# Kernel optimization log

Measured on AMD Instinct MI355X. Metric: run time of the kernel, lower is better.

The kernel has to match this reference:

```python
import jax, jax.numpy as jnp
import numpy as np

N = 100000        # nodes
E = 1600000       # edges (avg degree 16)
F_IN = 128        # num_node_features
H = 64            # hidden_channels
F_EDGE = 8        # num_edge_features (output dim per edge)


def setup_inputs() -> dict:
    key = jax.random.key(0)
    ks = jax.random.split(key, 9)
    x = jax.random.normal(ks[0], (N, F_IN), dtype=jnp.float32)
    edge_index = jax.random.randint(ks[1], (2, E), 0, N, dtype=jnp.int32)
    s = 0.05
    W1 = jax.random.normal(ks[2], (F_IN, H), jnp.float32) * s
    b1 = jnp.zeros((H,), jnp.float32)
    W2 = jax.random.normal(ks[3], (H, H), jnp.float32) * s
    b2 = jnp.zeros((H,), jnp.float32)
    Wl = jax.random.normal(ks[4], (2 * H, F_EDGE), jnp.float32) * s
    bl = jnp.zeros((F_EDGE,), jnp.float32)
    return {"x": x, "edge_index": edge_index,
            "W1": W1, "b1": b1, "W2": W2, "b2": b2, "Wl": Wl, "bl": bl}


def gcn_conv(x, W, b, row, col, n):
    # GCNConv: h = D^{-1/2} (A + I) D^{-1/2} (x W) + b
    h = x @ W
    sl = jnp.arange(n, dtype=row.dtype)          # self-loops
    r = jnp.concatenate([row, sl])
    c = jnp.concatenate([col, sl])
    ones = jnp.ones(r.shape[0], dtype=h.dtype)
    deg = jax.ops.segment_sum(ones, c, num_segments=n)      # in-degree incl. self-loop
    dinv = jax.lax.rsqrt(jnp.maximum(deg, 1e-12))
    norm = dinv[r] * dinv[c]                                 # symmetric normalization
    agg = jax.ops.segment_sum(norm[:, None] * h[r], c, num_segments=n)
    return agg + b


def reference(x, edge_index, W1, b1, W2, b2, Wl, bl):
    row, col = edge_index[0], edge_index[1]
    h = jax.nn.relu(gcn_conv(x, W1, b1, row, col, N))
    # dropout p=0.5 is identity at inference (training=False)
    h = jax.nn.relu(gcn_conv(h, W2, b2, row, col, N))
    x_i = h[row]                                  # [E, H]
    x_j = h[col]                                  # [E, H]
    return jnp.concatenate([x_i, x_j], axis=-1) @ Wl + bl   # [E, F_EDGE]
```

## Files before the change

kernel.cpp:

```cpp
#include <hip/hip_runtime.h>
#include <hip/hip_bf16.h>

static constexpr int NN  = 100000;
static constexpr int NE  = 1600000;
static constexpr int FIN = 128;
static constexpr int HD  = 64;

static constexpr int NB    = 256;
static constexpr int NPB   = 392;
static constexpr int EPB   = NE / NB;
static constexpr unsigned long long DIV392_MAGIC = 43826197ULL;

typedef __attribute__((ext_vector_type(8))) short bf16x8;
typedef __attribute__((ext_vector_type(4))) float f32x4;

__device__ __forceinline__ float bf2f(unsigned short u) {
    return __uint_as_float(((unsigned int)u) << 16);
}
__device__ __forceinline__ unsigned short f2bf(float f) {
    __hip_bfloat16 hb = __float2bfloat16(f);
    return *(unsigned short*)&hb;
}
__device__ __forceinline__ int bucket_of(int c) {
    return (int)(((unsigned long long)(unsigned int)c * DIV392_MAGIC) >> 34);
}

__global__ __launch_bounds__(256) void k_detect(const unsigned short* __restrict__ xu,
                                                int* __restrict__ flag) {
    __shared__ int sd[256];
    int t = threadIdx.x;
    int cnt = 0;
    for (int k = t; k < 4096; k += 256) {
        unsigned short u = xu[2 * k];
        int ex = (u >> 7) & 0xFF;
        cnt += (ex >= 110 && ex <= 135) ? 1 : 0;
    }
    sd[t] = cnt;
    __syncthreads();
    for (int off = 128; off > 0; off >>= 1) {
        if (t < off) sd[t] += sd[t + off];
        __syncthreads();
    }
    if (t == 0) flag[0] = (sd[0] >= 2048) ? 1 : 0;
}

__device__ __forceinline__ float load_in(const void* p, size_t i, int isbf) {
    return isbf ? bf2f(((const unsigned short*)p)[i]) : ((const float*)p)[i];
}

__global__ __launch_bounds__(256) void k_hist(const int* __restrict__ col, int* __restrict__ hist) {
    __shared__ int h[4][NB];
    int t = threadIdx.x, w = t >> 6;
#pragma unroll
    for (int r = 0; r < 4; ++r) h[r][t] = 0;
    __syncthreads();
    int base = blockIdx.x * EPB;
    for (int e = base + t; e < base + EPB; e += 256)
        atomicAdd(&h[w][bucket_of(col[e])], 1);
    __syncthreads();
    hist[t * NB + blockIdx.x] = h[0][t] + h[1][t] + h[2][t] + h[3][t];
}

__global__ __launch_bounds__(256) void k_gscan1(int* __restrict__ a, int* __restrict__ bsums) {
    __shared__ int sd[256];
    int t = threadIdx.x;
    int base = blockIdx.x * 1024 + t * 4;
    int v0 = a[base], v1 = a[base + 1], v2 = a[base + 2], v3 = a[base + 3];
    int tsum = v0 + v1 + v2 + v3;
    sd[t] = tsum;
    __syncthreads();
    for (int off = 1; off < 256; off <<= 1) {
        int tmp = (t >= off) ? sd[t - off] : 0;
        __syncthreads();
        sd[t] += tmp;
        __syncthreads();
    }
    int run = sd[t] - tsum;
    a[base] = run; run += v0;
    a[base + 1] = run; run += v1;
    a[base + 2] = run; run += v2;
    a[base + 3] = run;
    if (t == 255) bsums[blockIdx.x] = sd[t];
}

__global__ __launch_bounds__(256) void k_gscan2(int* __restrict__ bsums) {
    __shared__ int sd[256];
    int t = threadIdx.x;
    int v = (t < 64) ? bsums[t] : 0;
    sd[t] = v;
    __syncthreads();
    for (int off = 1; off < 256; off <<= 1) {
        int tmp = (t >= off) ? sd[t - off] : 0;
        __syncthreads();
        sd[t] += tmp;
        __syncthreads();
    }
    if (t < 64) bsums[t] = sd[t] - v;
}

__global__ __launch_bounds__(256) void k_binfill(const int* __restrict__ row, const int* __restrict__ col,
                                                 const int* __restrict__ histS, const int* __restrict__ bsums,
                                                 int* __restrict__ csr_tmp) {
    __shared__ int cur[NB];
    int t = threadIdx.x;
    cur[t] = histS[t * NB + blockIdx.x] + bsums[t >> 2];
    __syncthreads();
    int base = blockIdx.x * EPB;
    for (int e = base + t; e < base + EPB; e += 256) {
        int r = row[e], c = col[e];
        int b = bucket_of(c);
        int p = atomicAdd(&cur[b], 1);
        csr_tmp[p] = r | ((c - b * NPB) << 17);
    }
}

__global__ __launch_bounds__(256) void k_bsort(const int* __restrict__ csr_tmp,
                                               const int* __restrict__ histS,
                                               const int* __restrict__ bsums,
                                               int* __restrict__ csr_src,
                                               int* __restrict__ start,
                                               float* __restrict__ dinv) {
    __shared__ int cnt[512];
    __shared__ int cur[512];
    int t = threadIdx.x;
    int k = blockIdx.x;
    int S = histS[k * NB] + bsums[k >> 2];
    int E = (k < NB - 1) ? (histS[(k + 1) * NB] + bsums[(k + 1) >> 2]) : NE;
    int nbase = k * NPB;
    cnt[t] = 0; cnt[t + 256] = 0;
    __syncthreads();
    for (int e = S + t; e < E; e += 256)
        atomicAdd(&cnt[csr_tmp[e] >> 17], 1);
    __syncthreads();
    int rc0 = cnt[t], rc1 = cnt[t + 256];
    for (int d = 1; d < 512; d <<= 1) {
        int idx = (t + 1) * (d << 1) - 1;
        if (idx < 512) cnt[idx] += cnt[idx - d];
        __syncthreads();
    }
    if (t == 0) cnt[511] = 0;
    __syncthreads();
    for (int d = 256; d >= 1; d >>= 1) {
        int idx = (t + 1) * (d << 1) - 1;
        if (idx < 512) { int tmp = cnt[idx - d]; cnt[idx - d] = cnt[idx]; cnt[idx] += tmp; }
        __syncthreads();
    }
    int n0 = nbase + t;
    if (n0 < NN) {
        start[n0] = S + cnt[t] + rc0;
        dinv[n0] = rsqrtf((float)(rc0 + 1));
    }
    int li = t + 256;
    int n1 = nbase + li;
    if (li < NPB && n1 < NN) {
        start[n1] = S + cnt[li] + rc1;
        dinv[n1] = rsqrtf((float)(rc1 + 1));
    }
    cur[t] = cnt[t]; cur[t + 256] = cnt[t + 256];
    __syncthreads();
    for (int e = S + t; e < E; e += 256) {
        int u = csr_tmp[e];
        int p = atomicAdd(&cur[u >> 17], 1);
        csr_src[S + p] = u & 0x1FFFF;
    }
}

template <int K, bool XDUAL>
__global__ __launch_bounds__(256) void k_gemm_mfma(const void* __restrict__ X,
                                                   const void* __restrict__ W,
                                                   const float* __restrict__ dinv,
                                                   unsigned short* __restrict__ T0,
                                                   unsigned short* __restrict__ T1,
                                                   const int* __restrict__ flag) {
    constexpr int KT = K / 32;
    __shared__ unsigned short Bs[KT * 4 * 64 * 8];
    int isbf = flag[0];
    for (int tup = threadIdx.x; tup < KT * 4 * 64; tup += 256) {
        int l  = tup & 63;
        int nt = (tup >> 6) & 3;
        int kt = tup >> 8;
        int n  = nt * 16 + (l & 15);
        int kb = kt * 32 + (l >> 4) * 8;
        unsigned short tmp[8];
#pragma unroll
        for (int j = 0; j < 8; ++j) tmp[j] = f2bf(load_in(W, (size_t)(kb + j) * HD + n, isbf));
        *((uint4*)&Bs[(size_t)tup * 8]) = *((const uint4*)tmp);
    }
    __syncthreads();
    int wave = threadIdx.x >> 6, lane = threadIdx.x & 63;
    int quad = lane >> 4, m = lane & 15;
    int row0 = blockIdx.x * 64 + wave * 16;
    int row  = row0 + m;
    int rowc = (row < NN) ? row : (NN - 1);
    bool xf32 = XDUAL && (isbf == 0);
    const char* xrow = (const char*)X + (size_t)rowc * K * (xf32 ? 4 : 2);
    f32x4 acc[4];
#pragma unroll
    for (int nt = 0; nt < 4; ++nt) acc[nt] = (f32x4){0.f, 0.f, 0.f, 0.f};
#pragma unroll
    for (int kt = 0; kt < KT; ++kt) {
        bf16x8 a;
        if (!xf32) {
            a = *((const bf16x8*)(xrow + (size_t)(kt * 32 + quad * 8) * 2));
        } else {
            const float4* fp = (const float4*)(xrow + (size_t)(kt * 32 + quad * 8) * 4);
            float4 u0 = fp[0], u1 = fp[1];
            unsigned short tmp[8] = {f2bf(u0.x), f2bf(u0.y), f2bf(u0.z), f2bf(u0.w),
                                     f2bf(u1.x), f2bf(u1.y), f2bf(u1.z), f2bf(u1.w)};
            a = *((const bf16x8*)tmp);
        }
#pragma unroll
        for (int nt = 0; nt < 4; ++nt) {
            bf16x8 b = *((const bf16x8*)&Bs[(size_t)((kt * 4 + nt) * 64 + lane) * 8]);
            acc[nt] = __builtin_amdgcn_mfma_f32_16x16x32_bf16(a, b, acc[nt], 0, 0, 0);
        }
    }
#pragma unroll
    for (int r = 0; r < 4; ++r) {
        int orow = row0 + quad * 4 + r;
        if (orow < NN) {
            float sc = dinv[orow];
#pragma unroll
            for (int nt = 0; nt < 4; ++nt) {
                unsigned short* Th = (nt >= 2) ? T1 : T0;
                Th[(size_t)orow * 32 + (nt & 1) * 16 + m] = f2bf(acc[nt][r] * sc);
            }
        }
    }
}

__global__ __launch_bounds__(256) void k_agg_half(const unsigned short* __restrict__ Th,
                                                  unsigned short* __restrict__ Hout,
                                                  const int* __restrict__ endOff,
                                                  const int* __restrict__ csr_src,
                                                  const float* __restrict__ dinv,
                                                  const void* __restrict__ bias,
                                                  const int* __restrict__ flag,
                                                  int half) {
    int isbf = flag[0];
    int lane = threadIdx.x & 63, wave = threadIdx.x >> 6;
    int g  = lane >> 3;
    int fl = (lane & 7) * 4;
    int i = blockIdx.x * 32 + wave * 8 + g;
    int end = endOff[i];
    int beg = (i == 0) ? 0 : endOff[i - 1];
    float a0, a1, a2, a3;
    {
        ushort4 t = *((const ushort4*)(Th + (size_t)i * 32 + fl));
        a0 = bf2f(t.x); a1 = bf2f(t.y); a2 = bf2f(t.z); a3 = bf2f(t.w);
    }
    int k = beg;
    for (; k + 3 < end; k += 4) {
        int s0 = csr_src[k], s1 = csr_src[k + 1], s2 = csr_src[k + 2], s3 = csr_src[k + 3];
        ushort4 t0 = *((const ushort4*)(Th + (size_t)s0 * 32 + fl));
        ushort4 t1 = *((const ushort4*)(Th + (size_t)s1 * 32 + fl));
        ushort4 t2 = *((const ushort4*)(Th + (size_t)s2 * 32 + fl));
        ushort4 t3 = *((const ushort4*)(Th + (size_t)s3 * 32 + fl));
        a0 += bf2f(t0.x) + bf2f(t1.x) + bf2f(t2.x) + bf2f(t3.x);
        a1 += bf2f(t0.y) + bf2f(t1.y) + bf2f(t2.y) + bf2f(t3.y);
        a2 += bf2f(t0.z) + bf2f(t1.z) + bf2f(t2.z) + bf2f(t3.z);
        a3 += bf2f(t0.w) + bf2f(t1.w) + bf2f(t2.w) + bf2f(t3.w);
    }
    for (; k < end; ++k) {
        int s = csr_src[k];
        ushort4 t = *((const ushort4*)(Th + (size_t)s * 32 + fl));
        a0 += bf2f(t.x); a1 += bf2f(t.y); a2 += bf2f(t.z); a3 += bf2f(t.w);
    }
    float di = dinv[i];
    int fg = half * 32 + fl;
    float b0 = load_in(bias, fg + 0, isbf), b1 = load_in(bias, fg + 1, isbf);
    float b2 = load_in(bias, fg + 2, isbf), b3 = load_in(bias, fg + 3, isbf);
    ushort4 o;
    o.x = f2bf(fmaxf(fmaf(di, a0, b0), 0.f));
    o.y = f2bf(fmaxf(fmaf(di, a1, b1), 0.f));
    o.z = f2bf(fmaxf(fmaf(di, a2, b2), 0.f));
    o.w = f2bf(fmaxf(fmaf(di, a3, b3), 0.f));
    *((ushort4*)(Hout + (size_t)i * HD + fg)) = o;
}

__global__ __launch_bounds__(256) void k_pgemm(const __hip_bfloat16* __restrict__ H,
                                               const void* __restrict__ Wl,
                                               const void* __restrict__ bl,
                                               unsigned short* __restrict__ P,
                                               const int* __restrict__ flag) {
    int isbf = flag[0];
    int wave = threadIdx.x >> 6, lane = threadIdx.x & 63;
    int quad = lane >> 4, m = lane & 15;
    bf16x8 bfr[2];
#pragma unroll
    for (int kt = 0; kt < 2; ++kt) {
        unsigned short tmp[8];
#pragma unroll
        for (int j = 0; j < 8; ++j) {
            int kk = kt * 32 + quad * 8 + j;
            float w = (m < 8) ? load_in(Wl, (size_t)kk * 8 + m, isbf)
                              : load_in(Wl, (size_t)(64 + kk) * 8 + (m - 8), isbf);
            tmp[j] = f2bf(w);
        }
        bfr[kt] = *((const bf16x8*)tmp);
    }
    float binit = (m < 8) ? load_in(bl, m, isbf) : 0.f;
    int row0 = blockIdx.x * 64 + wave * 16;
    int row  = row0 + m;
    int rowc = (row < NN) ? row : (NN - 1);
    const __hip_bfloat16* hrow = H + (size_t)rowc * HD;
    bf16x8 x0 = *((const bf16x8*)(hrow + quad * 8));
    bf16x8 x1 = *((const bf16x8*)(hrow + 32 + quad * 8));
    f32x4 acc = (f32x4){binit, binit, binit, binit};
    acc = __builtin_amdgcn_mfma_f32_16x16x32_bf16(x0, bfr[0], acc, 0, 0, 0);
    acc = __builtin_amdgcn_mfma_f32_16x16x32_bf16(x1, bfr[1], acc, 0, 0, 0);
#pragma unroll
    for (int r = 0; r < 4; ++r) {
        int orow = row0 + quad * 4 + r;
        if (orow < NN) P[(size_t)orow * 16 + m] = f2bf(acc[r]);
    }
}

__global__ __launch_bounds__(256) void k_edge_add(const unsigned short* __restrict__ P,
                                                  const int* __restrict__ erow,
                                                  const int* __restrict__ ecol,
                                                  void* __restrict__ out,
                                                  const int* __restrict__ flag) {
    int isbf = flag[0];
    int e = blockIdx.x * 256 + threadIdx.x;
    int i = erow[e], j = ecol[e];
    ushort4 r0 = *((const ushort4*)(P + (size_t)i * 16));
    ushort4 r1 = *((const ushort4*)(P + (size_t)i * 16 + 4));
    ushort4 c0 = *((const ushort4*)(P + (size_t)j * 16 + 8));
    ushort4 c1 = *((const ushort4*)(P + (size_t)j * 16 + 12));
    float v[8] = {bf2f(r0.x) + bf2f(c0.x), bf2f(r0.y) + bf2f(c0.y),
                  bf2f(r0.z) + bf2f(c0.z), bf2f(r0.w) + bf2f(c0.w),
                  bf2f(r1.x) + bf2f(c1.x), bf2f(r1.y) + bf2f(c1.y),
                  bf2f(r1.z) + bf2f(c1.z), bf2f(r1.w) + bf2f(c1.w)};
    if (isbf) {
        union { unsigned short h[8]; uint4 u; } p;
#pragma unroll
        for (int o = 0; o < 8; ++o) p.h[o] = f2bf(v[o]);
        *((uint4*)((__hip_bfloat16*)out + (size_t)e * 8)) = p.u;
    } else {
        float* op = (float*)out + (size_t)e * 8;
        ((float4*)op)[0] = make_float4(v[0], v[1], v[2], v[3]);
        ((float4*)op)[1] = make_float4(v[4], v[5], v[6], v[7]);
    }
}

extern "C" void kernel_launch(void* const* d_in, const int* in_sizes, int n_in,
                              void* d_out, int out_size, void* d_ws, size_t ws_size,
                              hipStream_t stream) {
    const void* x  = d_in[0];
    const int*  ei = (const int*)d_in[1];
    const void* W1 = d_in[2];
    const void* b1 = d_in[3];
    const void* W2 = d_in[4];
    const void* b2 = d_in[5];
    const void* Wl = d_in[6];
    const void* bl = d_in[7];
    const int* row = ei;
    const int* col = ei + NE;

    char* ws = (char*)d_ws;
    int*   flag    = (int*)ws;    ws += 16;
    int*   hist    = (int*)ws;    ws += (size_t)NB * NB * 4;
    int*   bsums   = (int*)ws;    ws += 256 * 4;
    int*   start   = (int*)ws;    ws += (size_t)NN * 4;
    float* dinv    = (float*)ws;  ws += (size_t)NN * 4;
    int*   csr_tmp = (int*)ws;    ws += (size_t)NE * 4;
    int*   csr_src = (int*)ws;    ws += (size_t)NE * 4;
    unsigned short* T0 = (unsigned short*)ws;  ws += (size_t)NN * 32 * 2;
    unsigned short* T1 = (unsigned short*)ws;  ws += (size_t)NN * 32 * 2;
    __hip_bfloat16* bufH = (__hip_bfloat16*)ws;  ws += (size_t)NN * HD * 2;
    unsigned short* P = (unsigned short*)ws;

    int gE   = (NE + 255) / 256;
    int gN32 = NN / 32;
    int gN64 = (NN + 63) / 64;

    k_detect<<<1, 256, 0, stream>>>((const unsigned short*)x, flag);
    k_hist   <<<NB, 256, 0, stream>>>(col, hist);
    k_gscan1 <<<64, 256, 0, stream>>>(hist, bsums);
    k_gscan2 <<<1, 256, 0, stream>>>(bsums);
    k_binfill<<<NB, 256, 0, stream>>>(row, col, hist, bsums, csr_tmp);
    k_bsort  <<<NB, 256, 0, stream>>>(csr_tmp, hist, bsums, csr_src, start, dinv);

    k_gemm_mfma<FIN, true><<<gN64, 256, 0, stream>>>(x, W1, dinv, T0, T1, flag);
    k_agg_half<<<gN32, 256, 0, stream>>>(T0, (unsigned short*)bufH, start, csr_src, dinv, b1, flag, 0);
    k_agg_half<<<gN32, 256, 0, stream>>>(T1, (unsigned short*)bufH, start, csr_src, dinv, b1, flag, 1);

    k_gemm_mfma<HD, false><<<gN64, 256, 0, stream>>>(bufH, W2, dinv, T0, T1, flag);
    k_agg_half<<<gN32, 256, 0, stream>>>(T0, (unsigned short*)bufH, start, csr_src, dinv, b2, flag, 0);
    k_agg_half<<<gN32, 256, 0, stream>>>(T1, (unsigned short*)bufH, start, csr_src, dinv, b2, flag, 1);

    k_pgemm<<<gN64, 256, 0, stream>>>(bufH, Wl, bl, P, flag);
    k_edge_add<<<gE, 256, 0, stream>>>(P, row, col, d_out, flag);
}
```

Baseline: 335.0 us.

## Fuse aggregation with following GEMMs and merge small setup kernels

Folds the dtype-detect kernel into the histogram kernel and replaces the block-sum scan kernel with a small in-block scan inside the binfill and bsort kernels. Each GCN aggregation now gathers full 64-wide rows in a single pass instead of two half passes. The aggregated rows are staged in LDS and fed directly to the next MFMA GEMM (W2 or the edge projection), so the intermediate hidden buffer never goes through global memory. This cuts kernel launches and global round trips, at the cost of redundant bsums scans in every block and wider per-lane gathers.

```diff
diff --git a/kernel.cpp b/kernel.cpp
--- a/kernel.cpp
+++ b/kernel.cpp
@@ -25,30 +25,13 @@
     return (int)(((unsigned long long)(unsigned int)c * DIV392_MAGIC) >> 34);
 }
 
-__global__ __launch_bounds__(256) void k_detect(const unsigned short* __restrict__ xu,
-                                                int* __restrict__ flag) {
-    __shared__ int sd[256];
-    int t = threadIdx.x;
-    int cnt = 0;
-    for (int k = t; k < 4096; k += 256) {
-        unsigned short u = xu[2 * k];
-        int ex = (u >> 7) & 0xFF;
-        cnt += (ex >= 110 && ex <= 135) ? 1 : 0;
-    }
-    sd[t] = cnt;
-    __syncthreads();
-    for (int off = 128; off > 0; off >>= 1) {
-        if (t < off) sd[t] += sd[t + off];
-        __syncthreads();
-    }
-    if (t == 0) flag[0] = (sd[0] >= 2048) ? 1 : 0;
-}
-
 __device__ __forceinline__ float load_in(const void* p, size_t i, int isbf) {
     return isbf ? bf2f(((const unsigned short*)p)[i]) : ((const float*)p)[i];
 }
 
-__global__ __launch_bounds__(256) void k_hist(const int* __restrict__ col, int* __restrict__ hist) {
+__global__ __launch_bounds__(256) void k_hist(const int* __restrict__ col, int* __restrict__ hist,
+                                              const unsigned short* __restrict__ xu,
+                                              int* __restrict__ flag) {
     __shared__ int h[4][NB];
     int t = threadIdx.x, w = t >> 6;
 #pragma unroll
@@ -59,6 +42,22 @@
         atomicAdd(&h[w][bucket_of(col[e])], 1);
     __syncthreads();
     hist[t * NB + blockIdx.x] = h[0][t] + h[1][t] + h[2][t] + h[3][t];
+    if (blockIdx.x == 0) {
+        __syncthreads();
+        int cnt = 0;
+        for (int k = t; k < 4096; k += 256) {
+            unsigned short u = xu[2 * k];
+            int ex = (u >> 7) & 0xFF;
+            cnt += (ex >= 110 && ex <= 135) ? 1 : 0;
+        }
+        h[0][t] = cnt;
+        __syncthreads();
+        for (int off = 128; off > 0; off >>= 1) {
+            if (t < off) h[0][t] += h[0][t + off];
+            __syncthreads();
+        }
+        if (t == 0) flag[0] = (h[0][0] >= 2048) ? 1 : 0;
+    }
 }
 
 __global__ __launch_bounds__(256) void k_gscan1(int* __restrict__ a, int* __restrict__ bsums) {
@@ -83,27 +82,30 @@
     if (t == 255) bsums[blockIdx.x] = sd[t];
 }
 
-__global__ __launch_bounds__(256) void k_gscan2(int* __restrict__ bsums) {
-    __shared__ int sd[256];
+__device__ __forceinline__ void scan_bsums(const int* __restrict__ bsumsRaw, int* sb) {
     int t = threadIdx.x;
-    int v = (t < 64) ? bsums[t] : 0;
-    sd[t] = v;
-    __syncthreads();
-    for (int off = 1; off < 256; off <<= 1) {
-        int tmp = (t >= off) ? sd[t - off] : 0;
-        __syncthreads();
-        sd[t] += tmp;
-        __syncthreads();
-    }
-    if (t < 64) bsums[t] = sd[t] - v;
+    int myv = 0;
+    if (t < 64) { myv = bsumsRaw[t]; sb[t] = myv; }
+    __syncthreads();
+    for (int off = 1; off < 64; off <<= 1) {
+        int v = (t < 64 && t >= off) ? sb[t - off] : 0;
+        __syncthreads();
+        if (t < 64) sb[t] += v;
+        __syncthreads();
+    }
+    if (t < 64) sb[t] -= myv;
+    __syncthreads();
 }
 
 __global__ __launch_bounds__(256) void k_binfill(const int* __restrict__ row, const int* __restrict__ col,
-                                                 const int* __restrict__ histS, const int* __restrict__ bsums,
+                                                 const int* __restrict__ histS,
+                                                 const int* __restrict__ bsumsRaw,
                                                  int* __restrict__ csr_tmp) {
     __shared__ int cur[NB];
+    __shared__ int sb[64];
     int t = threadIdx.x;
-    cur[t] = histS[t * NB + blockIdx.x] + bsums[t >> 2];
+    scan_bsums(bsumsRaw, sb);
+    cur[t] = histS[t * NB + blockIdx.x] + sb[t >> 2];
     __syncthreads();
     int base = blockIdx.x * EPB;
     for (int e = base + t; e < base + EPB; e += 256) {
@@ -116,18 +118,20 @@
 
 __global__ __launch_bounds__(256) void k_bsort(const int* __restrict__ csr_tmp,
                                                const int* __restrict__ histS,
-                                               const int* __restrict__ bsums,
+                                               const int* __restrict__ bsumsRaw,
                                                int* __restrict__ csr_src,
                                                int* __restrict__ start,
                                                float* __restrict__ dinv) {
     __shared__ int cnt[512];
     __shared__ int cur[512];
+    __shared__ int sb[64];
     int t = threadIdx.x;
     int k = blockIdx.x;
-    int S = histS[k * NB] + bsums[k >> 2];
-    int E = (k < NB - 1) ? (histS[(k + 1) * NB] + bsums[(k + 1) >> 2]) : NE;
+    cnt[t] = 0; cnt[t + 256] = 0;
+    scan_bsums(bsumsRaw, sb);
+    int S = histS[k * NB] + sb[k >> 2];
+    int E = (k < NB - 1) ? (histS[(k + 1) * NB] + sb[(k + 1) >> 2]) : NE;
     int nbase = k * NPB;
-    cnt[t] = 0; cnt[t + 256] = 0;
     __syncthreads();
     for (int e = S + t; e < E; e += 256)
         atomicAdd(&cnt[csr_tmp[e] >> 17], 1);
@@ -169,8 +173,7 @@
 __global__ __launch_bounds__(256) void k_gemm_mfma(const void* __restrict__ X,
                                                    const void* __restrict__ W,
                                                    const float* __restrict__ dinv,
-                                                   unsigned short* __restrict__ T0,
-                                                   unsigned short* __restrict__ T1,
+                                                   unsigned short* __restrict__ T,
                                                    const int* __restrict__ flag) {
     constexpr int KT = K / 32;
     __shared__ unsigned short Bs[KT * 4 * 64 * 8];
@@ -221,70 +224,118 @@
         if (orow < NN) {
             float sc = dinv[orow];
 #pragma unroll
-            for (int nt = 0; nt < 4; ++nt) {
-                unsigned short* Th = (nt >= 2) ? T1 : T0;
-                Th[(size_t)orow * 32 + (nt & 1) * 16 + m] = f2bf(acc[nt][r] * sc);
-            }
-        }
-    }
-}
-
-__global__ __launch_bounds__(256) void k_agg_half(const unsigned short* __restrict__ Th,
-                                                  unsigned short* __restrict__ Hout,
+            for (int nt = 0; nt < 4; ++nt)
+                T[(size_t)orow * 64 + nt * 16 + m] = f2bf(acc[nt][r] * sc);
+        }
+    }
+}
+
+__device__ __forceinline__ void agg_to_lds(const unsigned short* __restrict__ T,
+                                           const int* __restrict__ endOff,
+                                           const int* __restrict__ csr_src,
+                                           const float* __restrict__ dinv,
+                                           const void* __restrict__ bias, int isbf,
+                                           unsigned short (*hS)[72], int i0) {
+    int lane = threadIdx.x & 63, wave = threadIdx.x >> 6;
+    int g  = lane >> 3;
+    int fl = (lane & 7) * 8;
+    int li = wave * 8 + g;
+    int i  = i0 + li;
+    int end = endOff[i];
+    int beg = (i == 0) ? 0 : endOff[i - 1];
+    union U { uint4 u; unsigned short s[8]; };
+    float a[8];
+    {
+        U t; t.u = *((const uint4*)(T + (size_t)i * 64 + fl));
+#pragma unroll
+        for (int j = 0; j < 8; ++j) a[j] = bf2f(t.s[j]);
+    }
+    int k = beg;
+    for (; k + 3 < end; k += 4) {
+        int s0 = csr_src[k], s1 = csr_src[k + 1], s2 = csr_src[k + 2], s3 = csr_src[k + 3];
+        U t0, t1, t2, t3;
+        t0.u = *((const uint4*)(T + (size_t)s0 * 64 + fl));
+        t1.u = *((const uint4*)(T + (size_t)s1 * 64 + fl));
+        t2.u = *((const uint4*)(T + (size_t)s2 * 64 + fl));
+        t3.u = *((const uint4*)(T + (size_t)s3 * 64 + fl));
+#pragma unroll
+        for (int j = 0; j < 8; ++j)
+            a[j] += bf2f(t0.s[j]) + bf2f(t1.s[j]) + bf2f(t2.s[j]) + bf2f(t3.s[j]);
+    }
+    for (; k < end; ++k) {
+        int s = csr_src[k];
+        U t; t.u = *((const uint4*)(T + (size_t)s * 64 + fl));
+#pragma unroll
+        for (int j = 0; j < 8; ++j) a[j] += bf2f(t.s[j]);
+    }
+    float di = dinv[i];
+    U o;
+#pragma unroll
+    for (int j = 0; j < 8; ++j)
+        o.s[j] = f2bf(fmaxf(fmaf(di, a[j], load_in(bias, fl + j, isbf)), 0.f));
+    *((uint4*)&hS[li][fl]) = o.u;
+}
+
+__global__ __launch_bounds__(256) void k_agg_gemm(const unsigned short* __restrict__ T,
                                                   const int* __restrict__ endOff,
                                                   const int* __restrict__ csr_src,
                                                   const float* __restrict__ dinv,
                                                   const void* __restrict__ bias,
+                                                  const void* __restrict__ W2,
                                                   const int* __restrict__ flag,
-                                                  int half) {
+                                                  unsigned short* __restrict__ Tb) {
+    __shared__ unsigned short hS[32][72];
+    __shared__ unsigned short Bs[2 * 4 * 64 * 8];
     int isbf = flag[0];
-    int lane = threadIdx.x & 63, wave = threadIdx.x >> 6;
-    int g  = lane >> 3;
-    int fl = (lane & 7) * 4;
-    int i = blockIdx.x * 32 + wave * 8 + g;
-    int end = endOff[i];
-    int beg = (i == 0) ? 0 : endOff[i - 1];
-    float a0, a1, a2, a3;
-    {
-        ushort4 t = *((const ushort4*)(Th + (size_t)i * 32 + fl));
-        a0 = bf2f(t.x); a1 = bf2f(t.y); a2 = bf2f(t.z); a3 = bf2f(t.w);
-    }
-    int k = beg;
-    for (; k + 3 < end; k += 4) {
-        int s0 = csr_src[k], s1 = csr_src[k + 1], s2 = csr_src[k + 2], s3 = csr_src[k + 3];
-        ushort4 t0 = *((const ushort4*)(Th + (size_t)s0 * 32 + fl));
-        ushort4 t1 = *((const ushort4*)(Th + (size_t)s1 * 32 + fl));
-        ushort4 t2 = *((const ushort4*)(Th + (size_t)s2 * 32 + fl));
-        ushort4 t3 = *((const ushort4*)(Th + (size_t)s3 * 32 + fl));
-        a0 += bf2f(t0.x) + bf2f(t1.x) + bf2f(t2.x) + bf2f(t3.x);
-        a1 += bf2f(t0.y) + bf2f(t1.y) + bf2f(t2.y) + bf2f(t3.y);
-        a2 += bf2f(t0.z) + bf2f(t1.z) + bf2f(t2.z) + bf2f(t3.z);
-        a3 += bf2f(t0.w) + bf2f(t1.w) + bf2f(t2.w) + bf2f(t3.w);
-    }
-    for (; k < end; ++k) {
-        int s = csr_src[k];
-        ushort4 t = *((const ushort4*)(Th + (size_t)s * 32 + fl));
-        a0 += bf2f(t.x); a1 += bf2f(t.y); a2 += bf2f(t.z); a3 += bf2f(t.w);
-    }
-    float di = dinv[i];
-    int fg = half * 32 + fl;
-    float b0 = load_in(bias, fg + 0, isbf), b1 = load_in(bias, fg + 1, isbf);
-    float b2 = load_in(bias, fg + 2, isbf), b3 = load_in(bias, fg + 3, isbf);
-    ushort4 o;
-    o.x = f2bf(fmaxf(fmaf(di, a0, b0), 0.f));
-    o.y = f2bf(fmaxf(fmaf(di, a1, b1), 0.f));
-    o.z = f2bf(fmaxf(fmaf(di, a2, b2), 0.f));
-    o.w = f2bf(fmaxf(fmaf(di, a3, b3), 0.f));
-    *((ushort4*)(Hout + (size_t)i * HD + fg)) = o;
-}
-
-__global__ __launch_bounds__(256) void k_pgemm(const __hip_bfloat16* __restrict__ H,
-                                               const void* __restrict__ Wl,
-                                               const void* __restrict__ bl,
-                                               unsigned short* __restrict__ P,
-                                               const int* __restrict__ flag) {
+    for (int tup = threadIdx.x; tup < 512; tup += 256) {
+        int l  = tup & 63;
+        int nt = (tup >> 6) & 3;
+        int kt = tup >> 8;
+        int n  = nt * 16 + (l & 15);
+        int kb = kt * 32 + (l >> 4) * 8;
+        unsigned short tmp[8];
+#pragma unroll
+        for (int j = 0; j < 8; ++j) tmp[j] = f2bf(load_in(W2, (size_t)(kb + j) * HD + n, isbf));
+        *((uint4*)&Bs[(size_t)tup * 8]) = *((const uint4*)tmp);
+    }
+    int i0 = blockIdx.x * 32;
+    agg_to_lds(T, endOff, csr_src, dinv, bias, isbf, hS, i0);
+    __syncthreads();
+    int wave = threadIdx.x >> 6, lane = threadIdx.x & 63;
+    int quad = lane >> 4, m = lane & 15;
+    int tile = wave >> 1;
+    int nb   = (wave & 1) * 2;
+    f32x4 acc0 = (f32x4){0.f, 0.f, 0.f, 0.f};
+    f32x4 acc1 = (f32x4){0.f, 0.f, 0.f, 0.f};
+#pragma unroll
+    for (int kt = 0; kt < 2; ++kt) {
+        bf16x8 a  = *((const bf16x8*)&hS[tile * 16 + m][kt * 32 + quad * 8]);
+        bf16x8 b0 = *((const bf16x8*)&Bs[(size_t)((kt * 4 + nb) * 64 + lane) * 8]);
+        bf16x8 b1 = *((const bf16x8*)&Bs[(size_t)((kt * 4 + nb + 1) * 64 + lane) * 8]);
+        acc0 = __builtin_amdgcn_mfma_f32_16x16x32_bf16(a, b0, acc0, 0, 0, 0);
+        acc1 = __builtin_amdgcn_mfma_f32_16x16x32_bf16(a, b1, acc1, 0, 0, 0);
+    }
+#pragma unroll
+    for (int r = 0; r < 4; ++r) {
+        int orow = i0 + tile * 16 + quad * 4 + r;
+        float sc = dinv[orow];
+        Tb[(size_t)orow * 64 + nb * 16 + m]       = f2bf(acc0[r] * sc);
+        Tb[(size_t)orow * 64 + (nb + 1) * 16 + m] = f2bf(acc1[r] * sc);
+    }
+}
+
+__global__ __launch_bounds__(256) void k_agg_pgemm(const unsigned short* __restrict__ T,
+                                                   const int* __restrict__ endOff,
+                                                   const int* __restrict__ csr_src,
+                                                   const float* __restrict__ dinv,
+                                                   const void* __restrict__ bias,
+                                                   const void* __restrict__ Wl,
+                                                   const void* __restrict__ bl,
+                                                   const int* __restrict__ flag,
+                                                   unsigned short* __restrict__ P) {
+    __shared__ unsigned short hS[32][72];
     int isbf = flag[0];
-    int wave = threadIdx.x >> 6, lane = threadIdx.x & 63;
+    int lane = threadIdx.x & 63;
     int quad = lane >> 4, m = lane & 15;
     bf16x8 bfr[2];
 #pragma unroll
@@ -300,19 +351,22 @@
         bfr[kt] = *((const bf16x8*)tmp);
     }
     float binit = (m < 8) ? load_in(bl, m, isbf) : 0.f;
-    int row0 = blockIdx.x * 64 + wave * 16;
-    int row  = row0 + m;
-    int rowc = (row < NN) ? row : (NN - 1);
-    const __hip_bfloat16* hrow = H + (size_t)rowc * HD;
-    bf16x8 x0 = *((const bf16x8*)(hrow + quad * 8));
-    bf16x8 x1 = *((const bf16x8*)(hrow + 32 + quad * 8));
-    f32x4 acc = (f32x4){binit, binit, binit, binit};
-    acc = __builtin_amdgcn_mfma_f32_16x16x32_bf16(x0, bfr[0], acc, 0, 0, 0);
-    acc = __builtin_amdgcn_mfma_f32_16x16x32_bf16(x1, bfr[1], acc, 0, 0, 0);
-#pragma unroll
-    for (int r = 0; r < 4; ++r) {
-        int orow = row0 + quad * 4 + r;
-        if (orow < NN) P[(size_t)orow * 16 + m] = f2bf(acc[r]);
+    int i0 = blockIdx.x * 32;
+    agg_to_lds(T, endOff, csr_src, dinv, bias, isbf, hS, i0);
+    __syncthreads();
+    int wave = threadIdx.x >> 6;
+    if (wave < 2) {
+        f32x4 acc = (f32x4){binit, binit, binit, binit};
+#pragma unroll
+        for (int kt = 0; kt < 2; ++kt) {
+            bf16x8 a = *((const bf16x8*)&hS[wave * 16 + m][kt * 32 + quad * 8]);
+            acc = __builtin_amdgcn_mfma_f32_16x16x32_bf16(a, bfr[kt], acc, 0, 0, 0);
+        }
+#pragma unroll
+        for (int r = 0; r < 4; ++r) {
+            int orow = i0 + wave * 16 + quad * 4 + r;
+            P[(size_t)orow * 16 + m] = f2bf(acc[r]);
+        }
     }
 }
 
@@ -366,30 +420,24 @@
     float* dinv    = (float*)ws;  ws += (size_t)NN * 4;
     int*   csr_tmp = (int*)ws;    ws += (size_t)NE * 4;
     int*   csr_src = (int*)ws;    ws += (size_t)NE * 4;
-    unsigned short* T0 = (unsigned short*)ws;  ws += (size_t)NN * 32 * 2;
-    unsigned short* T1 = (unsigned short*)ws;  ws += (size_t)NN * 32 * 2;
-    __hip_bfloat16* bufH = (__hip_bfloat16*)ws;  ws += (size_t)NN * HD * 2;
-    unsigned short* P = (unsigned short*)ws;
+    unsigned short* T  = (unsigned short*)ws;  ws += (size_t)NN * 64 * 2;
+    unsigned short* Tb = (unsigned short*)ws;  ws += (size_t)NN * 64 * 2;
+    unsigned short* P  = (unsigned short*)ws;
 
     int gE   = (NE + 255) / 256;
     int gN32 = NN / 32;
     int gN64 = (NN + 63) / 64;
 
-    k_detect<<<1, 256, 0, stream>>>((const unsigned short*)x, flag);
-    k_hist   <<<NB, 256, 0, stream>>>(col, hist);
+    k_hist   <<<NB, 256, 0, stream>>>(col, hist, (const unsigned short*)x, flag);
     k_gscan1 <<<64, 256, 0, stream>>>(hist, bsums);
-    k_gscan2 <<<1, 256, 0, stream>>>(bsums);
     k_binfill<<<NB, 256, 0, stream>>>(row, col, hist, bsums, csr_tmp);
     k_bsort  <<<NB, 256, 0, stream>>>(csr_tmp, hist, bsums, csr_src, start, dinv);
 
-    k_gemm_mfma<FIN, true><<<gN64, 256, 0, stream>>>(x, W1, dinv, T0, T1, flag);
-    k_agg_half<<<gN32, 256, 0, stream>>>(T0, (unsigned short*)bufH, start, csr_src, dinv, b1, flag, 0);
-    k_agg_half<<<gN32, 256, 0, stream>>>(T1, (unsigned short*)bufH, start, csr_src, dinv, b1, flag, 1);
-
-    k_gemm_mfma<HD, false><<<gN64, 256, 0, stream>>>(bufH, W2, dinv, T0, T1, flag);
-    k_agg_half<<<gN32, 256, 0, stream>>>(T0, (unsigned short*)bufH, start, csr_src, dinv, b2, flag, 0);
-    k_agg_half<<<gN32, 256, 0, stream>>>(T1, (unsigned short*)bufH, start, csr_src, dinv, b2, flag, 1);
-
-    k_pgemm<<<gN64, 256, 0, stream>>>(bufH, Wl, bl, P, flag);
-    k_edge_add<<<gE, 256, 0, stream>>>(P, row, col, d_out, flag);
-}
+    k_gemm_mfma<FIN, true><<<gN64, 256, 0, stream>>>(x, W1, dinv, T, flag);
+
+    k_agg_gemm <<<gN32, 256, 0, stream>>>(T, start, csr_src, dinv, b1, W2, flag, Tb);
+
+    k_agg_pgemm<<<gN32, 256, 0, stream>>>(Tb, start, csr_src, dinv, b2, Wl, bl, flag, P);
+
+    k_edge_add <<<gE, 256, 0, stream>>>(P, row, col, d_out, flag);
+}
```

New measurement: 293.0 us. -12.5%, faster.
